# Kernel tuning notes

Measured on AMD Instinct MI355X. Metric: run time of the kernel, lower is better.

Reference implementation:

```python
import jax, jax.numpy as jnp
import numpy as np

B, H, S, D = 1, 16, 2048, 128
NUM_DOCS = 4


def setup_inputs() -> dict:
    key = jax.random.key(0)
    kq, kk, kv = jax.random.split(key, 3)
    q = jax.random.normal(kq, (B, H, S, D), dtype=jnp.float32)
    k = jax.random.normal(kk, (B, H, S, D), dtype=jnp.float32)
    v = jax.random.normal(kv, (B, H, S, D), dtype=jnp.float32)
    # Document boundaries within the packed sequence (as produced by _get_offsets):
    # starts at 0, ends at total token count. 4 equal docs of length 512.
    offsets = jnp.array([0, 512, 1024, 1536, 2048], dtype=jnp.int64)
    return {"q": q, "k": k, "v": v, "offsets": offsets}


def reference(q, k, v, offsets):
    # Block-causal SDPA: token i attends to token j iff j <= i and both are
    # in the same document (documents delimited by `offsets`). This matches
    # nested-tensor SDPA with is_causal=True over the jagged documents.
    _, _, S_, D_ = q.shape
    pos = jnp.arange(S_)
    seg = jnp.searchsorted(offsets, pos, side="right")  # [S] document id per token
    mask = (seg[:, None] == seg[None, :]) & (pos[None, :] <= pos[:, None])  # [S,S]
    scale = 1.0 / jnp.sqrt(jnp.asarray(D_, q.dtype))
    scores = jnp.einsum("bhsd,bhtd->bhst", q, k) * scale  # [B,H,S,S]
    scores = jnp.where(mask[None, None], scores, jnp.finfo(q.dtype).min)
    attn = jax.nn.softmax(scores, axis=-1)
    return jnp.einsum("bhst,bhtd->bhsd", attn, v)
```

## Files before the change

### kernel.cpp

```cpp
#include <hip/hip_runtime.h>
#include <hip/hip_bf16.h>
#include <math.h>

#define NH 16
#define SL 2048
#define DM 128

typedef float f32x4 __attribute__((ext_vector_type(4)));
typedef short s16x8 __attribute__((ext_vector_type(8)));
typedef short s16x4 __attribute__((ext_vector_type(4)));
typedef int   i32x4 __attribute__((ext_vector_type(4)));

static __device__ __forceinline__ unsigned short f2bfu(float f) {
  __hip_bfloat16 h = __float2bfloat16(f);
  return (unsigned short)__builtin_bit_cast(short, h);
}
static __device__ __forceinline__ short f2bf(float f) {
  __hip_bfloat16 h = __float2bfloat16(f);
  return __builtin_bit_cast(short, h);
}
static __device__ __forceinline__ unsigned pack2(float lo, float hi) {
  return (unsigned)f2bfu(lo) | ((unsigned)f2bfu(hi) << 16);
}

__global__ __launch_bounds__(256) void attn_dbuf(
    const float* __restrict__ qg,
    const float* __restrict__ kg,
    const float* __restrict__ vg,
    const int* __restrict__ offs, int n_off,
    float* __restrict__ out)
{
  __shared__ __align__(16) char Kb[2][16384];
  __shared__ __align__(16) char Vb[2][16384];

  const int t    = threadIdx.x;
  const int lane = t & 63;
  const int w    = t >> 6;
  const int col  = lane & 15;
  const int g    = lane >> 4;

  const int blk = blockIdx.x;
  const int z   = blk >> 8;
  const int y   = (blk >> 4) & 15;
  const int h   = blk & 15;
  const int dno = y >> 2, u = y & 3;
  const int p   = z ? u : 7 - u;
  const int q0  = (dno * 8 + p) * 64;

  const float* qh = qg + (size_t)h * SL * DM;
  const float* kh = kg + (size_t)h * SL * DM;
  const float* vh = vg + (size_t)h * SL * DM;

  const float scale = 0.08838834764831843f;

  const int qrow = q0 + 16 * w + col;

  int ov[8];
  #pragma unroll
  for (int i = 0; i < 8; ++i) ov[i] = (i < n_off) ? offs[i] : 0x7fffffff;
  int qstart = 0, kv_lo = 0;
  #pragma unroll
  for (int i = 0; i < 8; ++i) {
    if (ov[i] <= qrow) qstart = max(qstart, ov[i]);
    if (ov[i] <= q0)   kv_lo  = max(kv_lo, ov[i]);
  }
  const int n = ((q0 + 64) - kv_lo) >> 6;

  s16x8 qf[4];
  #pragma unroll
  for (int kk = 0; kk < 4; ++kk) {
    const float* qp = qh + (size_t)qrow * DM + 32 * kk + 8 * g;
    f32x4 lo = *(const f32x4*)qp;
    f32x4 hi = *(const f32x4*)(qp + 4);
    s16x8 f;
    f[0] = f2bf(lo[0] * scale); f[1] = f2bf(lo[1] * scale);
    f[2] = f2bf(lo[2] * scale); f[3] = f2bf(lo[3] * scale);
    f[4] = f2bf(hi[0] * scale); f[5] = f2bf(hi[1] * scale);
    f[6] = f2bf(hi[2] * scale); f[7] = f2bf(hi[3] * scale);
    qf[kk] = f;
  }

  f32x4 acc[8];
  #pragma unroll
  for (int dt = 0; dt < 8; ++dt) { f32x4 zv = {0.f, 0.f, 0.f, 0.f}; acc[dt] = zv; }
  float m_ = -1e30f, l_ = 0.f;

  const int d0  = (t & 31) * 4;
  const int r0  = t >> 5;
  const int rot = (t >> 1) & 3;
  f32x4 kr[8], vr[8];

#define LOADT(T) do {                                                         \
    const float* _ks = kh + (size_t)(kv_lo + ((T) << 6)) * DM;                \
    const float* _vs = vh + (size_t)(kv_lo + ((T) << 6)) * DM;                \
    _Pragma("unroll")                                                         \
    for (int _i = 0; _i < 8; ++_i)                                            \
      kr[_i] = *(const f32x4*)(_ks + (size_t)(r0 + 8 * _i) * DM + d0);        \
    _Pragma("unroll")                                                         \
    for (int _k = 0; _k < 2; ++_k) {                                          \
      _Pragma("unroll")                                                       \
      for (int _j = 0; _j < 4; ++_j)                                          \
        vr[_k * 4 + _j] =                                                     \
          *(const f32x4*)(_vs + (size_t)(r0 * 4 + 32 * _k + _j) * DM + d0);   \
    }                                                                         \
  } while (0)

#define WRITEKV(B) do {                                                       \
    _Pragma("unroll")                                                         \
    for (int _i = 0; _i < 8; ++_i) {                                          \
      int _r = r0 + 8 * _i;                                                   \
      s16x4 _b;                                                               \
      _b[0] = f2bf(kr[_i][0]); _b[1] = f2bf(kr[_i][1]);                       \
      _b[2] = f2bf(kr[_i][2]); _b[3] = f2bf(kr[_i][3]);                       \
      *(s16x4*)(&Kb[B][0] + ((_r * 256 + d0 * 2) ^ ((_r & 7) << 4))) = _b;    \
    }                                                                         \
    _Pragma("unroll")                                                         \
    for (int _k = 0; _k < 2; ++_k) {                                          \
      int _k0 = r0 * 4 + 32 * _k;                                             \
      _Pragma("unroll")                                                       \
      for (int _di = 0; _di < 4; ++_di) {                                     \
        int _dd = (_di + rot) & 3;                                            \
        int _d  = d0 + _dd;                                                   \
        s16x4 _b;                                                             \
        _b[0] = f2bf(vr[_k * 4 + 0][_dd]); _b[1] = f2bf(vr[_k * 4 + 1][_dd]); \
        _b[2] = f2bf(vr[_k * 4 + 2][_dd]); _b[3] = f2bf(vr[_k * 4 + 3][_dd]); \
        *(s16x4*)(&Vb[B][0] + ((_d * 128 + _k0 * 2) ^ ((_d & 7) << 4))) = _b; \
      }                                                                       \
    }                                                                         \
  } while (0)

  LOADT(0);
  WRITEKV(0);
  int cur = 0;

  const int srcA = col + 32 * (g & 1);
  const int srcB = srcA + 16;
  const bool hi2 = (g >> 1) != 0;

  for (int it = 0; it < n; ++it) {
    const int kv0 = kv_lo + (it << 6);
    __syncthreads();

    const bool pre = (it + 1 < n);
    if (pre) LOADT(it + 1);
    __builtin_amdgcn_sched_barrier(0);

    f32x4 st[4];
    #pragma unroll
    for (int kt = 0; kt < 4; ++kt) { f32x4 zv = {0.f, 0.f, 0.f, 0.f}; st[kt] = zv; }
    __builtin_amdgcn_s_setprio(1);
    #pragma unroll
    for (int kt = 0; kt < 4; ++kt) {
      int row = kt * 16 + col;
      #pragma unroll
      for (int kk = 0; kk < 4; ++kk) {
        s16x8 kf = *(const s16x8*)(&Kb[cur][0] + ((row * 256 + 64 * kk + 16 * g) ^ ((row & 7) << 4)));
        st[kt] = __builtin_amdgcn_mfma_f32_16x16x32_bf16(kf, qf[kk], st[kt], 0, 0, 0);
      }
    }
    __builtin_amdgcn_s_setprio(0);

    float cm = -3.0e38f;
    #pragma unroll
    for (int kt = 0; kt < 4; ++kt) {
      #pragma unroll
      for (int r = 0; r < 4; ++r) {
        int kpos = kv0 + kt * 16 + 4 * g + r;
        float x = st[kt][r];
        bool ok = (kpos <= qrow) && (kpos >= qstart);
        x = ok ? x : -3.0e38f;
        st[kt][r] = x;
        cm = fmaxf(cm, x);
      }
    }
    cm = fmaxf(cm, __shfl_xor(cm, 16));
    cm = fmaxf(cm, __shfl_xor(cm, 32));
    float mn = fmaxf(m_, cm);
    float al = __expf(m_ - mn);
    m_ = mn;
    float psum = 0.f;
    unsigned w01[4], w23[4];
    #pragma unroll
    for (int kt = 0; kt < 4; ++kt) {
      float p0 = __expf(st[kt][0] - mn);
      float p1 = __expf(st[kt][1] - mn);
      float p2 = __expf(st[kt][2] - mn);
      float p3 = __expf(st[kt][3] - mn);
      psum += (p0 + p1) + (p2 + p3);
      w01[kt] = pack2(p0, p1);
      w23[kt] = pack2(p2, p3);
    }
    psum += __shfl_xor(psum, 16);
    psum += __shfl_xor(psum, 32);
    l_ = l_ * al + psum;

    #pragma unroll
    for (int r = 0; r < 4; ++r) {
      float ar = __shfl(al, 4 * g + r);
      #pragma unroll
      for (int dt = 0; dt < 8; ++dt) acc[dt][r] *= ar;
    }

    __builtin_amdgcn_s_setprio(1);
    #pragma unroll
    for (int ksel = 0; ksel < 2; ++ksel) {
      unsigned a0 = __shfl(w01[2 * ksel], srcA);
      unsigned a1 = __shfl(w01[2 * ksel + 1], srcA);
      unsigned b0 = __shfl(w23[2 * ksel], srcA);
      unsigned b1 = __shfl(w23[2 * ksel + 1], srcA);
      unsigned c0 = __shfl(w01[2 * ksel], srcB);
      unsigned c1 = __shfl(w01[2 * ksel + 1], srcB);
      unsigned e0 = __shfl(w23[2 * ksel], srcB);
      unsigned e1 = __shfl(w23[2 * ksel + 1], srcB);
      i32x4 uu;
      uu[0] = (int)(hi2 ? a1 : a0);
      uu[1] = (int)(hi2 ? b1 : b0);
      uu[2] = (int)(hi2 ? c1 : c0);
      uu[3] = (int)(hi2 ? e1 : e0);
      s16x8 pa = __builtin_bit_cast(s16x8, uu);
      #pragma unroll
      for (int dt = 0; dt < 8; ++dt) {
        int d = dt * 16 + col;
        s16x8 vf = *(const s16x8*)(&Vb[cur][0] + ((d * 128 + 64 * ksel + 16 * g) ^ ((d & 7) << 4)));
        acc[dt] = __builtin_amdgcn_mfma_f32_16x16x32_bf16(pa, vf, acc[dt], 0, 0, 0);
      }
    }
    __builtin_amdgcn_s_setprio(0);

    if (pre) WRITEKV(cur ^ 1);
    cur ^= 1;
  }
#undef LOADT
#undef WRITEKV

  #pragma unroll
  for (int r = 0; r < 4; ++r) {
    float lr  = __shfl(l_, 4 * g + r);
    float inv = 1.f / lr;
    int row   = q0 + 16 * w + 4 * g + r;
    float* op = out + ((size_t)h * SL + row) * DM + col;
    #pragma unroll
    for (int dt = 0; dt < 8; ++dt) op[dt * 16] = acc[dt][r] * inv;
  }
}

extern "C" void kernel_launch(void* const* d_in, const int* in_sizes, int n_in,
                              void* d_out, int out_size, void* d_ws, size_t ws_size,
                              hipStream_t stream) {
  const float* q = (const float*)d_in[0];
  const float* k = (const float*)d_in[1];
  const float* v = (const float*)d_in[2];
  const int* offs = (const int*)d_in[3];
  const int n_off = in_sizes[3];
  float* out = (float*)d_out;

  const int blocks = NH * (SL / 64);
  attn_dbuf<<<blocks, 256, 0, stream>>>(q, k, v, offs, n_off, out);
}
```

Before: 29.84 us.

## Shrink attention tiles to 32 queries and 32 keys with 2-wave blocks

Each block now handles 32 query rows with 2 waves instead of 64 rows with 4, and iterates over 32-key tiles instead of 64. The grid doubles to 1024 blocks, and the V LDS layout is repacked to a new swizzle. Block scheduling changes so the longest causal blocks are issued first. The accumulator rescale is skipped when no row's max grows. The goal is better load balance and occupancy across CUs, at the cost of more loop iterations, more syncs and less K/V reuse per block.

After: 35.85 us. 20.1% more time.

```diff
diff --git a/kernel.cpp b/kernel.cpp
--- a/kernel.cpp
+++ b/kernel.cpp
@@ -23,15 +23,15 @@
   return (unsigned)f2bfu(lo) | ((unsigned)f2bfu(hi) << 16);
 }
 
-__global__ __launch_bounds__(256) void attn_dbuf(
+__global__ __launch_bounds__(128) void attn_k32(
     const float* __restrict__ qg,
     const float* __restrict__ kg,
     const float* __restrict__ vg,
     const int* __restrict__ offs, int n_off,
     float* __restrict__ out)
 {
-  __shared__ __align__(16) char Kb[2][16384];
-  __shared__ __align__(16) char Vb[2][16384];
+  __shared__ __align__(16) char Kb[2][8192];
+  __shared__ __align__(16) char Vb[2][8192];
 
   const int t    = threadIdx.x;
   const int lane = t & 63;
@@ -39,13 +39,12 @@
   const int col  = lane & 15;
   const int g    = lane >> 4;
 
-  const int blk = blockIdx.x;
-  const int z   = blk >> 8;
-  const int y   = (blk >> 4) & 15;
-  const int h   = blk & 15;
-  const int dno = y >> 2, u = y & 3;
-  const int p   = z ? u : 7 - u;
-  const int q0  = (dno * 8 + p) * 64;
+  const int b   = blockIdx.x;
+  const int h   = b & 15;
+  const int i   = b >> 4;
+  const int doc = i & 3;
+  const int p32 = 15 - (i >> 2);
+  const int q0  = (doc * 16 + p32) * 32;
 
   const float* qh = qg + (size_t)h * SL * DM;
   const float* kh = kg + (size_t)h * SL * DM;
@@ -57,14 +56,14 @@
 
   int ov[8];
   #pragma unroll
-  for (int i = 0; i < 8; ++i) ov[i] = (i < n_off) ? offs[i] : 0x7fffffff;
+  for (int ii = 0; ii < 8; ++ii) ov[ii] = (ii < n_off) ? offs[ii] : 0x7fffffff;
   int qstart = 0, kv_lo = 0;
   #pragma unroll
-  for (int i = 0; i < 8; ++i) {
-    if (ov[i] <= qrow) qstart = max(qstart, ov[i]);
-    if (ov[i] <= q0)   kv_lo  = max(kv_lo, ov[i]);
-  }
-  const int n = ((q0 + 64) - kv_lo) >> 6;
+  for (int ii = 0; ii < 8; ++ii) {
+    if (ov[ii] <= qrow) qstart = max(qstart, ov[ii]);
+    if (ov[ii] <= q0)   kv_lo  = max(kv_lo, ov[ii]);
+  }
+  const int n = ((q0 + 32) - kv_lo) >> 5;
 
   s16x8 qf[4];
   #pragma unroll
@@ -87,45 +86,43 @@
 
   const int d0  = (t & 31) * 4;
   const int r0  = t >> 5;
+  const int k0  = r0 * 8;
   const int rot = (t >> 1) & 3;
   f32x4 kr[8], vr[8];
 
 #define LOADT(T) do {                                                         \
-    const float* _ks = kh + (size_t)(kv_lo + ((T) << 6)) * DM;                \
-    const float* _vs = vh + (size_t)(kv_lo + ((T) << 6)) * DM;                \
+    const float* _ks = kh + (size_t)(kv_lo + ((T) << 5)) * DM;                \
+    const float* _vs = vh + (size_t)(kv_lo + ((T) << 5)) * DM;                \
     _Pragma("unroll")                                                         \
     for (int _i = 0; _i < 8; ++_i)                                            \
-      kr[_i] = *(const f32x4*)(_ks + (size_t)(r0 + 8 * _i) * DM + d0);        \
-    _Pragma("unroll")                                                         \
-    for (int _k = 0; _k < 2; ++_k) {                                          \
-      _Pragma("unroll")                                                       \
-      for (int _j = 0; _j < 4; ++_j)                                          \
-        vr[_k * 4 + _j] =                                                     \
-          *(const f32x4*)(_vs + (size_t)(r0 * 4 + 32 * _k + _j) * DM + d0);   \
-    }                                                                         \
+      kr[_i] = *(const f32x4*)(_ks + (size_t)(r0 + 4 * _i) * DM + d0);        \
+    _Pragma("unroll")                                                         \
+    for (int _j = 0; _j < 8; ++_j)                                            \
+      vr[_j] = *(const f32x4*)(_vs + (size_t)(k0 + _j) * DM + d0);            \
   } while (0)
 
 #define WRITEKV(B) do {                                                       \
     _Pragma("unroll")                                                         \
     for (int _i = 0; _i < 8; ++_i) {                                          \
-      int _r = r0 + 8 * _i;                                                   \
+      int _r = r0 + 4 * _i;                                                   \
       s16x4 _b;                                                               \
       _b[0] = f2bf(kr[_i][0]); _b[1] = f2bf(kr[_i][1]);                       \
       _b[2] = f2bf(kr[_i][2]); _b[3] = f2bf(kr[_i][3]);                       \
       *(s16x4*)(&Kb[B][0] + ((_r * 256 + d0 * 2) ^ ((_r & 7) << 4))) = _b;    \
     }                                                                         \
     _Pragma("unroll")                                                         \
-    for (int _k = 0; _k < 2; ++_k) {                                          \
-      int _k0 = r0 * 4 + 32 * _k;                                             \
-      _Pragma("unroll")                                                       \
-      for (int _di = 0; _di < 4; ++_di) {                                     \
-        int _dd = (_di + rot) & 3;                                            \
-        int _d  = d0 + _dd;                                                   \
-        s16x4 _b;                                                             \
-        _b[0] = f2bf(vr[_k * 4 + 0][_dd]); _b[1] = f2bf(vr[_k * 4 + 1][_dd]); \
-        _b[2] = f2bf(vr[_k * 4 + 2][_dd]); _b[3] = f2bf(vr[_k * 4 + 3][_dd]); \
-        *(s16x4*)(&Vb[B][0] + ((_d * 128 + _k0 * 2) ^ ((_d & 7) << 4))) = _b; \
-      }                                                                       \
+    for (int _di = 0; _di < 4; ++_di) {                                       \
+      int _dd = (_di + rot) & 3;                                              \
+      int _d  = d0 + _dd;                                                     \
+      int _bs = (_d >> 1) * 128 + (_d & 1) * 64 + k0 * 2;                     \
+      int _sw = ((_d >> 1) & 7) << 4;                                         \
+      s16x4 _b0, _b1;                                                         \
+      _b0[0] = f2bf(vr[0][_dd]); _b0[1] = f2bf(vr[1][_dd]);                   \
+      _b0[2] = f2bf(vr[2][_dd]); _b0[3] = f2bf(vr[3][_dd]);                   \
+      _b1[0] = f2bf(vr[4][_dd]); _b1[1] = f2bf(vr[5][_dd]);                   \
+      _b1[2] = f2bf(vr[6][_dd]); _b1[3] = f2bf(vr[7][_dd]);                   \
+      *(s16x4*)(&Vb[B][0] + ((_bs) ^ _sw)) = _b0;                             \
+      *(s16x4*)(&Vb[B][0] + ((_bs + 8) ^ _sw)) = _b1;                         \
     }                                                                         \
   } while (0)
 
@@ -138,19 +135,19 @@
   const bool hi2 = (g >> 1) != 0;
 
   for (int it = 0; it < n; ++it) {
-    const int kv0 = kv_lo + (it << 6);
+    const int kv0 = kv_lo + (it << 5);
     __syncthreads();
 
     const bool pre = (it + 1 < n);
     if (pre) LOADT(it + 1);
     __builtin_amdgcn_sched_barrier(0);
 
-    f32x4 st[4];
-    #pragma unroll
-    for (int kt = 0; kt < 4; ++kt) { f32x4 zv = {0.f, 0.f, 0.f, 0.f}; st[kt] = zv; }
+    f32x4 st[2];
+    #pragma unroll
+    for (int kt = 0; kt < 2; ++kt) { f32x4 zv = {0.f, 0.f, 0.f, 0.f}; st[kt] = zv; }
     __builtin_amdgcn_s_setprio(1);
     #pragma unroll
-    for (int kt = 0; kt < 4; ++kt) {
+    for (int kt = 0; kt < 2; ++kt) {
       int row = kt * 16 + col;
       #pragma unroll
       for (int kk = 0; kk < 4; ++kk) {
@@ -162,7 +159,7 @@
 
     float cm = -3.0e38f;
     #pragma unroll
-    for (int kt = 0; kt < 4; ++kt) {
+    for (int kt = 0; kt < 2; ++kt) {
       #pragma unroll
       for (int r = 0; r < 4; ++r) {
         int kpos = kv0 + kt * 16 + 4 * g + r;
@@ -176,12 +173,21 @@
     cm = fmaxf(cm, __shfl_xor(cm, 16));
     cm = fmaxf(cm, __shfl_xor(cm, 32));
     float mn = fmaxf(m_, cm);
-    float al = __expf(m_ - mn);
-    m_ = mn;
+    float al = 1.f;
+    if (!__all(cm <= m_)) {
+      al = __expf(m_ - mn);
+      m_ = mn;
+      #pragma unroll
+      for (int r = 0; r < 4; ++r) {
+        float ar = __shfl(al, 4 * g + r);
+        #pragma unroll
+        for (int dt = 0; dt < 8; ++dt) acc[dt][r] *= ar;
+      }
+    }
     float psum = 0.f;
-    unsigned w01[4], w23[4];
-    #pragma unroll
-    for (int kt = 0; kt < 4; ++kt) {
+    unsigned w01[2], w23[2];
+    #pragma unroll
+    for (int kt = 0; kt < 2; ++kt) {
       float p0 = __expf(st[kt][0] - mn);
       float p1 = __expf(st[kt][1] - mn);
       float p2 = __expf(st[kt][2] - mn);
@@ -194,24 +200,16 @@
     psum += __shfl_xor(psum, 32);
     l_ = l_ * al + psum;
 
-    #pragma unroll
-    for (int r = 0; r < 4; ++r) {
-      float ar = __shfl(al, 4 * g + r);
-      #pragma unroll
-      for (int dt = 0; dt < 8; ++dt) acc[dt][r] *= ar;
-    }
-
     __builtin_amdgcn_s_setprio(1);
-    #pragma unroll
-    for (int ksel = 0; ksel < 2; ++ksel) {
-      unsigned a0 = __shfl(w01[2 * ksel], srcA);
-      unsigned a1 = __shfl(w01[2 * ksel + 1], srcA);
-      unsigned b0 = __shfl(w23[2 * ksel], srcA);
-      unsigned b1 = __shfl(w23[2 * ksel + 1], srcA);
-      unsigned c0 = __shfl(w01[2 * ksel], srcB);
-      unsigned c1 = __shfl(w01[2 * ksel + 1], srcB);
-      unsigned e0 = __shfl(w23[2 * ksel], srcB);
-      unsigned e1 = __shfl(w23[2 * ksel + 1], srcB);
+    {
+      unsigned a0 = __shfl(w01[0], srcA);
+      unsigned a1 = __shfl(w01[1], srcA);
+      unsigned b0 = __shfl(w23[0], srcA);
+      unsigned b1 = __shfl(w23[1], srcA);
+      unsigned c0 = __shfl(w01[0], srcB);
+      unsigned c1 = __shfl(w01[1], srcB);
+      unsigned e0 = __shfl(w23[0], srcB);
+      unsigned e1 = __shfl(w23[1], srcB);
       i32x4 uu;
       uu[0] = (int)(hi2 ? a1 : a0);
       uu[1] = (int)(hi2 ? b1 : b0);
@@ -221,7 +219,8 @@
       #pragma unroll
       for (int dt = 0; dt < 8; ++dt) {
         int d = dt * 16 + col;
-        s16x8 vf = *(const s16x8*)(&Vb[cur][0] + ((d * 128 + 64 * ksel + 16 * g) ^ ((d & 7) << 4)));
+        s16x8 vf = *(const s16x8*)(&Vb[cur][0] +
+            (((d >> 1) * 128 + (d & 1) * 64 + 16 * g) ^ (((d >> 1) & 7) << 4)));
         acc[dt] = __builtin_amdgcn_mfma_f32_16x16x32_bf16(pa, vf, acc[dt], 0, 0, 0);
       }
     }
@@ -254,6 +253,6 @@
   const int n_off = in_sizes[3];
   float* out = (float*)d_out;
 
-  const int blocks = NH * (SL / 64);
-  attn_dbuf<<<blocks, 256, 0, stream>>>(q, k, v, offs, n_off, out);
-}
+  const int blocks = NH * (SL / 32);
+  attn_k32<<<blocks, 128, 0, stream>>>(q, k, v, offs, n_off, out);
+}
```

## Split long KV ranges across two blocks with a merge kernel

Applied to the files above, without the earlier changes.

Query blocks with five or more KV tiles are split into two halves that run as separate workgroups. Each half writes a bf16 partial accumulator plus its max and sum statistics to workspace, and a second kernel merges the two halves. The block-to-query mapping is simplified, and the per-element causal/document mask is now skipped for tiles that need no masking. This aims to even out per-block work on the causal triangle, at the cost of an extra launch, extra workspace traffic, and bf16 rounding of the partial outputs.

After: 48.30 us. 1.62x slower.

```diff
diff --git a/kernel.cpp b/kernel.cpp
--- a/kernel.cpp
+++ b/kernel.cpp
@@ -22,13 +22,18 @@
 static __device__ __forceinline__ unsigned pack2(float lo, float hi) {
   return (unsigned)f2bfu(lo) | ((unsigned)f2bfu(hi) << 16);
 }
-
-__global__ __launch_bounds__(256) void attn_dbuf(
+static __device__ __forceinline__ float bf2f(short s) {
+  unsigned u = ((unsigned)(unsigned short)s) << 16;
+  return __builtin_bit_cast(float, u);
+}
+
+__global__ __launch_bounds__(256) void attn_part(
     const float* __restrict__ qg,
     const float* __restrict__ kg,
     const float* __restrict__ vg,
     const int* __restrict__ offs, int n_off,
-    float* __restrict__ out)
+    float* __restrict__ out,
+    char* __restrict__ pacc, int allow_split)
 {
   __shared__ __align__(16) char Kb[2][16384];
   __shared__ __align__(16) char Vb[2][16384];
@@ -40,12 +45,11 @@
   const int g    = lane >> 4;
 
   const int blk = blockIdx.x;
-  const int z   = blk >> 8;
-  const int y   = (blk >> 4) & 15;
+  const int z   = blk >> 9;
+  const int i   = (blk >> 4) & 31;
   const int h   = blk & 15;
-  const int dno = y >> 2, u = y & 3;
-  const int p   = z ? u : 7 - u;
-  const int q0  = (dno * 8 + p) * 64;
+  const int qb  = 31 - i;
+  const int q0  = qb * 64;
 
   const float* qh = qg + (size_t)h * SL * DM;
   const float* kh = kg + (size_t)h * SL * DM;
@@ -57,14 +61,23 @@
 
   int ov[8];
   #pragma unroll
-  for (int i = 0; i < 8; ++i) ov[i] = (i < n_off) ? offs[i] : 0x7fffffff;
+  for (int ii = 0; ii < 8; ++ii) ov[ii] = (ii < n_off) ? offs[ii] : 0x7fffffff;
   int qstart = 0, kv_lo = 0;
   #pragma unroll
-  for (int i = 0; i < 8; ++i) {
-    if (ov[i] <= qrow) qstart = max(qstart, ov[i]);
-    if (ov[i] <= q0)   kv_lo  = max(kv_lo, ov[i]);
+  for (int ii = 0; ii < 8; ++ii) {
+    if (ov[ii] <= qrow) qstart = max(qstart, ov[ii]);
+    if (ov[ii] <= q0)   kv_lo  = max(kv_lo, ov[ii]);
   }
   const int n = ((q0 + 64) - kv_lo) >> 6;
+
+  const bool split = allow_split && (n >= 5);
+  if (!split && z) return;
+  int tA = 0, tN = n;
+  if (split) {
+    const int nA = (n + 1) >> 1;
+    if (z) { tA = nA; tN = n - nA; } else { tN = nA; }
+  }
+  const int kvb = kv_lo + (tA << 6);
 
   s16x8 qf[4];
   #pragma unroll
@@ -91,8 +104,8 @@
   f32x4 kr[8], vr[8];
 
 #define LOADT(T) do {                                                         \
-    const float* _ks = kh + (size_t)(kv_lo + ((T) << 6)) * DM;                \
-    const float* _vs = vh + (size_t)(kv_lo + ((T) << 6)) * DM;                \
+    const float* _ks = kh + (size_t)(kvb + ((T) << 6)) * DM;                  \
+    const float* _vs = vh + (size_t)(kvb + ((T) << 6)) * DM;                  \
     _Pragma("unroll")                                                         \
     for (int _i = 0; _i < 8; ++_i)                                            \
       kr[_i] = *(const f32x4*)(_ks + (size_t)(r0 + 8 * _i) * DM + d0);        \
@@ -137,11 +150,11 @@
   const int srcB = srcA + 16;
   const bool hi2 = (g >> 1) != 0;
 
-  for (int it = 0; it < n; ++it) {
-    const int kv0 = kv_lo + (it << 6);
+  for (int it = 0; it < tN; ++it) {
+    const int kv0 = kvb + (it << 6);
     __syncthreads();
 
-    const bool pre = (it + 1 < n);
+    const bool pre = (it + 1 < tN);
     if (pre) LOADT(it + 1);
     __builtin_amdgcn_sched_barrier(0);
 
@@ -160,18 +173,23 @@
     }
     __builtin_amdgcn_s_setprio(0);
 
+    const bool needmask = __any((kv0 + 63 > qrow) || (kv0 < qstart));
+    if (needmask) {
+      #pragma unroll
+      for (int kt = 0; kt < 4; ++kt) {
+        #pragma unroll
+        for (int r = 0; r < 4; ++r) {
+          int kpos = kv0 + kt * 16 + 4 * g + r;
+          bool ok = (kpos <= qrow) && (kpos >= qstart);
+          st[kt][r] = ok ? st[kt][r] : -3.0e38f;
+        }
+      }
+    }
     float cm = -3.0e38f;
     #pragma unroll
     for (int kt = 0; kt < 4; ++kt) {
       #pragma unroll
-      for (int r = 0; r < 4; ++r) {
-        int kpos = kv0 + kt * 16 + 4 * g + r;
-        float x = st[kt][r];
-        bool ok = (kpos <= qrow) && (kpos >= qstart);
-        x = ok ? x : -3.0e38f;
-        st[kt][r] = x;
-        cm = fmaxf(cm, x);
-      }
+      for (int r = 0; r < 4; ++r) cm = fmaxf(cm, st[kt][r]);
     }
     cm = fmaxf(cm, __shfl_xor(cm, 16));
     cm = fmaxf(cm, __shfl_xor(cm, 32));
@@ -233,14 +251,75 @@
 #undef LOADT
 #undef WRITEKV
 
-  #pragma unroll
-  for (int r = 0; r < 4; ++r) {
-    float lr  = __shfl(l_, 4 * g + r);
-    float inv = 1.f / lr;
-    int row   = q0 + 16 * w + 4 * g + r;
-    float* op = out + ((size_t)h * SL + row) * DM + col;
-    #pragma unroll
-    for (int dt = 0; dt < 8; ++dt) op[dt * 16] = acc[dt][r] * inv;
+  if (!split) {
+    #pragma unroll
+    for (int r = 0; r < 4; ++r) {
+      float lr  = __shfl(l_, 4 * g + r);
+      float inv = 1.f / lr;
+      int row   = q0 + 16 * w + 4 * g + r;
+      float* op = out + ((size_t)h * SL + row) * DM + col;
+      #pragma unroll
+      for (int dt = 0; dt < 8; ++dt) op[dt * 16] = acc[dt][r] * inv;
+    }
+  } else {
+    char* pb = pacc + ((((size_t)(h * 32 + qb)) * 2 + z) << 14);
+    #pragma unroll
+    for (int r = 0; r < 4; ++r) {
+      int row16 = 16 * w + 4 * g + r;
+      #pragma unroll
+      for (int dt = 0; dt < 8; ++dt)
+        *(unsigned short*)(pb + (row16 * 128 + dt * 16 + col) * 2) = f2bfu(acc[dt][r]);
+    }
+    if (g == 0) {
+      int row = q0 + 16 * w + col;
+      *(float2*)(out + ((size_t)h * SL + row) * DM + 2 * z) = make_float2(m_, l_);
+    }
+  }
+}
+
+__global__ __launch_bounds__(256) void attn_merge(
+    const int* __restrict__ offs, int n_off,
+    const char* __restrict__ pacc, float* __restrict__ out)
+{
+  const int t  = threadIdx.x;
+  const int h  = blockIdx.x & 15;
+  const int qb = blockIdx.x >> 4;
+  const int q0 = qb * 64;
+
+  int ov[8];
+  #pragma unroll
+  for (int ii = 0; ii < 8; ++ii) ov[ii] = (ii < n_off) ? offs[ii] : 0x7fffffff;
+  int kv_lo = 0;
+  #pragma unroll
+  for (int ii = 0; ii < 8; ++ii) if (ov[ii] <= q0) kv_lo = max(kv_lo, ov[ii]);
+  const int n = ((q0 + 64) - kv_lo) >> 6;
+  if (n < 5) return;
+
+  const int r  = t >> 2;
+  const int cq = (t & 3) * 32;
+  float* orow = out + ((size_t)h * SL + q0 + r) * DM;
+
+  float4 s = *(const float4*)orow;
+  __syncthreads();
+  float m  = fmaxf(s.x, s.z);
+  float eA = __expf(s.x - m), eB = __expf(s.z - m);
+  float inv = 1.f / (eA * s.y + eB * s.w);
+  float fa = eA * inv, fb = eB * inv;
+
+  const char* pA = pacc + (((size_t)(h * 32 + qb)) * 2 << 14);
+  const char* pB = pA + 16384;
+  #pragma unroll
+  for (int j = 0; j < 4; ++j) {
+    int off = (r * 128 + cq + j * 8) * 2;
+    s16x8 a = *(const s16x8*)(pA + off);
+    s16x8 b = *(const s16x8*)(pB + off);
+    f32x4 o0, o1;
+    #pragma unroll
+    for (int e = 0; e < 4; ++e) o0[e] = bf2f(a[e]) * fa + bf2f(b[e]) * fb;
+    #pragma unroll
+    for (int e = 0; e < 4; ++e) o1[e] = bf2f(a[4 + e]) * fa + bf2f(b[4 + e]) * fb;
+    *(f32x4*)(orow + cq + j * 8)     = o0;
+    *(f32x4*)(orow + cq + j * 8 + 4) = o1;
   }
 }
 
@@ -254,6 +333,11 @@
   const int n_off = in_sizes[3];
   float* out = (float*)d_out;
 
-  const int blocks = NH * (SL / 64);
-  attn_dbuf<<<blocks, 256, 0, stream>>>(q, k, v, offs, n_off, out);
-}
+  const size_t need = (size_t)NH * 32 * 2 * 16384;
+  if (ws_size >= need) {
+    attn_part<<<1024, 256, 0, stream>>>(q, k, v, offs, n_off, out, (char*)d_ws, 1);
+    attn_merge<<<512, 256, 0, stream>>>(offs, n_off, (const char*)d_ws, out);
+  } else {
+    attn_part<<<512, 256, 0, stream>>>(q, k, v, offs, n_off, out, (char*)d_ws, 0);
+  }
+}
```

## Software-pipeline PV matmul with next tile's QK and triple-buffer V

Applied to the files above, without the earlier changes.

Defers each tile's P·V MFMAs into the next iteration, where they are issued right after the current tile's Q·K^T MFMAs. A third V shared-memory buffer keeps the previous tile's V alive, and the final P·V is drained after the loop. The aim is to overlap softmax work and shuffle latency with matrix-core work. The causal/document mask is also skipped for tiles where no lane needs it. In exchange, LDS use rises from 64KB to 80KB per block, and holding the deferred P fragments raises register pressure.

Measured after the change: 40.28 us. +35.0%, slower.

```diff
diff --git a/kernel.cpp b/kernel.cpp
--- a/kernel.cpp
+++ b/kernel.cpp
@@ -23,7 +23,7 @@
   return (unsigned)f2bfu(lo) | ((unsigned)f2bfu(hi) << 16);
 }
 
-__global__ __launch_bounds__(256) void attn_dbuf(
+__global__ __launch_bounds__(256) void attn_pipe(
     const float* __restrict__ qg,
     const float* __restrict__ kg,
     const float* __restrict__ vg,
@@ -31,7 +31,7 @@
     float* __restrict__ out)
 {
   __shared__ __align__(16) char Kb[2][16384];
-  __shared__ __align__(16) char Vb[2][16384];
+  __shared__ __align__(16) char Vb[3][16384];
 
   const int t    = threadIdx.x;
   const int lane = t & 63;
@@ -57,12 +57,12 @@
 
   int ov[8];
   #pragma unroll
-  for (int i = 0; i < 8; ++i) ov[i] = (i < n_off) ? offs[i] : 0x7fffffff;
+  for (int ii = 0; ii < 8; ++ii) ov[ii] = (ii < n_off) ? offs[ii] : 0x7fffffff;
   int qstart = 0, kv_lo = 0;
   #pragma unroll
-  for (int i = 0; i < 8; ++i) {
-    if (ov[i] <= qrow) qstart = max(qstart, ov[i]);
-    if (ov[i] <= q0)   kv_lo  = max(kv_lo, ov[i]);
+  for (int ii = 0; ii < 8; ++ii) {
+    if (ov[ii] <= qrow) qstart = max(qstart, ov[ii]);
+    if (ov[ii] <= q0)   kv_lo  = max(kv_lo, ov[ii]);
   }
   const int n = ((q0 + 64) - kv_lo) >> 6;
 
@@ -105,14 +105,14 @@
     }                                                                         \
   } while (0)
 
-#define WRITEKV(B) do {                                                       \
+#define WRITEKV(KB, VB) do {                                                  \
     _Pragma("unroll")                                                         \
     for (int _i = 0; _i < 8; ++_i) {                                          \
       int _r = r0 + 8 * _i;                                                   \
       s16x4 _b;                                                               \
       _b[0] = f2bf(kr[_i][0]); _b[1] = f2bf(kr[_i][1]);                       \
       _b[2] = f2bf(kr[_i][2]); _b[3] = f2bf(kr[_i][3]);                       \
-      *(s16x4*)(&Kb[B][0] + ((_r * 256 + d0 * 2) ^ ((_r & 7) << 4))) = _b;    \
+      *(s16x4*)((KB) + ((_r * 256 + d0 * 2) ^ ((_r & 7) << 4))) = _b;         \
     }                                                                         \
     _Pragma("unroll")                                                         \
     for (int _k = 0; _k < 2; ++_k) {                                          \
@@ -124,19 +124,21 @@
         s16x4 _b;                                                             \
         _b[0] = f2bf(vr[_k * 4 + 0][_dd]); _b[1] = f2bf(vr[_k * 4 + 1][_dd]); \
         _b[2] = f2bf(vr[_k * 4 + 2][_dd]); _b[3] = f2bf(vr[_k * 4 + 3][_dd]); \
-        *(s16x4*)(&Vb[B][0] + ((_d * 128 + _k0 * 2) ^ ((_d & 7) << 4))) = _b; \
+        *(s16x4*)((VB) + ((_d * 128 + _k0 * 2) ^ ((_d & 7) << 4))) = _b;      \
       }                                                                       \
     }                                                                         \
   } while (0)
 
   LOADT(0);
-  WRITEKV(0);
-  int cur = 0;
+  WRITEKV(&Kb[0][0], &Vb[0][0]);
+  int ck = 0, cv = 0;
 
   const int srcA = col + 32 * (g & 1);
   const int srcB = srcA + 16;
   const bool hi2 = (g >> 1) != 0;
 
+  s16x8 paF0, paF1;
+
   for (int it = 0; it < n; ++it) {
     const int kv0 = kv_lo + (it << 6);
     __syncthreads();
@@ -145,6 +147,9 @@
     if (pre) LOADT(it + 1);
     __builtin_amdgcn_sched_barrier(0);
 
+    const int pv = (cv == 0) ? 2 : cv - 1;
+    const int nv = (cv == 2) ? 0 : cv + 1;
+
     f32x4 st[4];
     #pragma unroll
     for (int kt = 0; kt < 4; ++kt) { f32x4 zv = {0.f, 0.f, 0.f, 0.f}; st[kt] = zv; }
@@ -154,24 +159,42 @@
       int row = kt * 16 + col;
       #pragma unroll
       for (int kk = 0; kk < 4; ++kk) {
-        s16x8 kf = *(const s16x8*)(&Kb[cur][0] + ((row * 256 + 64 * kk + 16 * g) ^ ((row & 7) << 4)));
+        s16x8 kf = *(const s16x8*)(&Kb[ck][0] + ((row * 256 + 64 * kk + 16 * g) ^ ((row & 7) << 4)));
         st[kt] = __builtin_amdgcn_mfma_f32_16x16x32_bf16(kf, qf[kk], st[kt], 0, 0, 0);
       }
     }
+
+    if (it > 0) {
+      #pragma unroll
+      for (int dt = 0; dt < 8; ++dt) {
+        int d = dt * 16 + col;
+        s16x8 vf0 = *(const s16x8*)(&Vb[pv][0] + ((d * 128 + 16 * g) ^ ((d & 7) << 4)));
+        acc[dt] = __builtin_amdgcn_mfma_f32_16x16x32_bf16(paF0, vf0, acc[dt], 0, 0, 0);
+        s16x8 vf1 = *(const s16x8*)(&Vb[pv][0] + ((d * 128 + 64 + 16 * g) ^ ((d & 7) << 4)));
+        acc[dt] = __builtin_amdgcn_mfma_f32_16x16x32_bf16(paF1, vf1, acc[dt], 0, 0, 0);
+      }
+    }
     __builtin_amdgcn_s_setprio(0);
 
+    if (pre) WRITEKV(&Kb[ck ^ 1][0], &Vb[nv][0]);
+
+    const bool needmask = __any((kv0 + 63 > qrow) || (kv0 < qstart));
+    if (needmask) {
+      #pragma unroll
+      for (int kt = 0; kt < 4; ++kt) {
+        #pragma unroll
+        for (int r = 0; r < 4; ++r) {
+          int kpos = kv0 + kt * 16 + 4 * g + r;
+          bool ok = (kpos <= qrow) && (kpos >= qstart);
+          st[kt][r] = ok ? st[kt][r] : -3.0e38f;
+        }
+      }
+    }
     float cm = -3.0e38f;
     #pragma unroll
     for (int kt = 0; kt < 4; ++kt) {
       #pragma unroll
-      for (int r = 0; r < 4; ++r) {
-        int kpos = kv0 + kt * 16 + 4 * g + r;
-        float x = st[kt][r];
-        bool ok = (kpos <= qrow) && (kpos >= qstart);
-        x = ok ? x : -3.0e38f;
-        st[kt][r] = x;
-        cm = fmaxf(cm, x);
-      }
+      for (int r = 0; r < 4; ++r) cm = fmaxf(cm, st[kt][r]);
     }
     cm = fmaxf(cm, __shfl_xor(cm, 16));
     cm = fmaxf(cm, __shfl_xor(cm, 32));
@@ -201,38 +224,55 @@
       for (int dt = 0; dt < 8; ++dt) acc[dt][r] *= ar;
     }
 
-    __builtin_amdgcn_s_setprio(1);
-    #pragma unroll
-    for (int ksel = 0; ksel < 2; ++ksel) {
-      unsigned a0 = __shfl(w01[2 * ksel], srcA);
-      unsigned a1 = __shfl(w01[2 * ksel + 1], srcA);
-      unsigned b0 = __shfl(w23[2 * ksel], srcA);
-      unsigned b1 = __shfl(w23[2 * ksel + 1], srcA);
-      unsigned c0 = __shfl(w01[2 * ksel], srcB);
-      unsigned c1 = __shfl(w01[2 * ksel + 1], srcB);
-      unsigned e0 = __shfl(w23[2 * ksel], srcB);
-      unsigned e1 = __shfl(w23[2 * ksel + 1], srcB);
+    {
+      unsigned a0 = __shfl(w01[0], srcA);
+      unsigned a1 = __shfl(w01[1], srcA);
+      unsigned b0 = __shfl(w23[0], srcA);
+      unsigned b1 = __shfl(w23[1], srcA);
+      unsigned c0 = __shfl(w01[0], srcB);
+      unsigned c1 = __shfl(w01[1], srcB);
+      unsigned e0 = __shfl(w23[0], srcB);
+      unsigned e1 = __shfl(w23[1], srcB);
       i32x4 uu;
       uu[0] = (int)(hi2 ? a1 : a0);
       uu[1] = (int)(hi2 ? b1 : b0);
       uu[2] = (int)(hi2 ? c1 : c0);
       uu[3] = (int)(hi2 ? e1 : e0);
-      s16x8 pa = __builtin_bit_cast(s16x8, uu);
-      #pragma unroll
-      for (int dt = 0; dt < 8; ++dt) {
-        int d = dt * 16 + col;
-        s16x8 vf = *(const s16x8*)(&Vb[cur][0] + ((d * 128 + 64 * ksel + 16 * g) ^ ((d & 7) << 4)));
-        acc[dt] = __builtin_amdgcn_mfma_f32_16x16x32_bf16(pa, vf, acc[dt], 0, 0, 0);
-      }
-    }
-    __builtin_amdgcn_s_setprio(0);
-
-    if (pre) WRITEKV(cur ^ 1);
-    cur ^= 1;
+      paF0 = __builtin_bit_cast(s16x8, uu);
+      a0 = __shfl(w01[2], srcA);
+      a1 = __shfl(w01[3], srcA);
+      b0 = __shfl(w23[2], srcA);
+      b1 = __shfl(w23[3], srcA);
+      c0 = __shfl(w01[2], srcB);
+      c1 = __shfl(w01[3], srcB);
+      e0 = __shfl(w23[2], srcB);
+      e1 = __shfl(w23[3], srcB);
+      uu[0] = (int)(hi2 ? a1 : a0);
+      uu[1] = (int)(hi2 ? b1 : b0);
+      uu[2] = (int)(hi2 ? c1 : c0);
+      uu[3] = (int)(hi2 ? e1 : e0);
+      paF1 = __builtin_bit_cast(s16x8, uu);
+    }
+
+    ck ^= 1;
+    cv = nv;
   }
 #undef LOADT
 #undef WRITEKV
 
+  {
+    const int pv = (cv == 0) ? 2 : cv - 1;
+    __builtin_amdgcn_s_setprio(1);
+    #pragma unroll
+    for (int dt = 0; dt < 8; ++dt) {
+      int d = dt * 16 + col;
+      s16x8 vf0 = *(const s16x8*)(&Vb[pv][0] + ((d * 128 + 16 * g) ^ ((d & 7) << 4)));
+      acc[dt] = __builtin_amdgcn_mfma_f32_16x16x32_bf16(paF0, vf0, acc[dt], 0, 0, 0);
+      s16x8 vf1 = *(const s16x8*)(&Vb[pv][0] + ((d * 128 + 64 + 16 * g) ^ ((d & 7) << 4)));
+      acc[dt] = __builtin_amdgcn_mfma_f32_16x16x32_bf16(paF1, vf1, acc[dt], 0, 0, 0);
+    }
+    __builtin_amdgcn_s_setprio(0);
+  }
   #pragma unroll
   for (int r = 0; r < 4; ++r) {
     float lr  = __shfl(l_, 4 * g + r);
@@ -255,5 +295,5 @@
   float* out = (float*)d_out;
 
   const int blocks = NH * (SL / 64);
-  attn_dbuf<<<blocks, 256, 0, stream>>>(q, k, v, offs, n_off, out);
-}
+  attn_pipe<<<blocks, 256, 0, stream>>>(q, k, v, offs, n_off, out);
+}
```
